# Performance work log

Measured on AMD Instinct MI355X. Metric: run time of the kernel, lower is better.

## Reference

```python
import jax, jax.numpy as jnp
import numpy as np

N_NODES = 100000
N_EDGES = 1600000
NODE_DIM = 128
HIDDEN_DIM = 128


def _sage_conv(x, src, dst, deg_inv, W_l, W_r, b):
    # PyG SAGEConv (aggr='mean', root_weight=True):
    #   out = lin_l(mean_{j in N(i)} x_j) + lin_r(x_i)
    msgs = x[src]                                             # [E, d_in] gather
    agg = jax.ops.segment_sum(msgs, dst, num_segments=N_NODES)  # [N, d_in]
    mean = agg * deg_inv[:, None]
    return mean @ W_l + x @ W_r + b


def setup_inputs() -> dict:
    key = jax.random.key(0)
    ks = jax.random.split(key, 9)
    x = jax.random.normal(ks[0], (N_NODES, NODE_DIM), dtype=jnp.float32)
    edge_index = jax.random.randint(ks[1], (2, N_EDGES), 0, N_NODES, dtype=jnp.int32)
    t = jnp.zeros((1,), dtype=jnp.float32)

    def glorot(k, fan_in, fan_out):
        s = (6.0 / (fan_in + fan_out)) ** 0.5
        return jax.random.uniform(k, (fan_in, fan_out), jnp.float32, -s, s)

    return {
        "t": t,
        "x": x,
        "edge_index": edge_index,
        "W1_l": glorot(ks[2], NODE_DIM, HIDDEN_DIM),
        "W1_r": glorot(ks[3], NODE_DIM, HIDDEN_DIM),
        "b1": jnp.zeros((HIDDEN_DIM,), jnp.float32),
        "W2_l": glorot(ks[4], HIDDEN_DIM, HIDDEN_DIM),
        "W2_r": glorot(ks[5], HIDDEN_DIM, HIDDEN_DIM),
        "b2": jnp.zeros((HIDDEN_DIM,), jnp.float32),
        "W3_l": glorot(ks[6], HIDDEN_DIM, NODE_DIM),
        "W3_r": glorot(ks[7], HIDDEN_DIM, NODE_DIM),
        "b3": jnp.zeros((NODE_DIM,), jnp.float32),
    }


def reference(t, x, edge_index, W1_l, W1_r, b1, W2_l, W2_r, b2, W3_l, W3_r, b3):
    src, dst = edge_index[0], edge_index[1]
    deg = jax.ops.segment_sum(jnp.ones((N_EDGES,), x.dtype), dst, num_segments=N_NODES)
    deg_inv = jnp.where(deg > 0, 1.0 / jnp.maximum(deg, 1.0), 0.0)

    h = jax.nn.relu(_sage_conv(x, src, dst, deg_inv, W1_l, W1_r, b1))
    h = jax.nn.relu(_sage_conv(h, src, dst, deg_inv, W2_l, W2_r, b2))
    dx_dt = _sage_conv(h, src, dst, deg_inv, W3_l, W3_r, b3)
    return dx_dt
```

## Files before the change

### kernel.cpp

```cpp
#include <hip/hip_runtime.h>

#define NN   100000
#define NE   1600000
#define DIM  128
#define NBKT 391
#define EPB  16384
#define NBLK 98
#define NTILES (NN / 16)
#define CASTB 12500
#define CWB   384


typedef short          s16x8 __attribute__((ext_vector_type(8)));
typedef unsigned short u16x8 __attribute__((ext_vector_type(8)));
typedef float          f32x4 __attribute__((ext_vector_type(4)));

__device__ __forceinline__ unsigned short f2b(float f) {
    unsigned u = __float_as_uint(f);
    unsigned r = ((u >> 16) & 1u) + 0x7FFFu;
    return (unsigned short)((u + r) >> 16);
}
__device__ __forceinline__ float b2f(unsigned short h) {
    return __uint_as_float(((unsigned)h) << 16);
}

__global__ void k_prep(const float* __restrict__ x, unsigned short* __restrict__ xb,
                       const int* __restrict__ dst, int* __restrict__ hist,
                       const float* __restrict__ W1l, const float* __restrict__ W1r,
                       const float* __restrict__ W2l, const float* __restrict__ W2r,
                       const float* __restrict__ W3l, const float* __restrict__ W3r,
                       unsigned short* __restrict__ Wt1, unsigned short* __restrict__ Wt2,
                       unsigned short* __restrict__ Wt3) {
    __shared__ int lh[NBKT];
    int t = threadIdx.x, b = blockIdx.x;
    if (b < NBLK) {
        for (int j = t; j < NBKT; j += 256) lh[j] = 0;
        __syncthreads();
        int base = b * EPB;
        int end = base + EPB; if (end > NE) end = NE;
        for (int i = base + t; i < end; i += 256) atomicAdd(&lh[dst[i] >> 8], 1);
        __syncthreads();
        for (int j = t; j < NBKT; j += 256) hist[j * NBLK + b] = lh[j];
    } else if (b < NBLK + CASTB) {
        int i = (b - NBLK) * 256 + t;
        float4 v = ((const float4*)x)[i];
        ushort4 o;
        o.x = f2b(v.x); o.y = f2b(v.y); o.z = f2b(v.z); o.w = f2b(v.w);
        ((ushort4*)xb)[i] = o;
    } else {
        int i = (b - NBLK - CASTB) * 256 + t;
        int L = i >> 15;
        int rem = i & 32767;
        int n = rem >> 8;
        int k = rem & 255;
        const float* Wl = (L == 0) ? W1l : (L == 1) ? W2l : W3l;
        const float* Wr = (L == 0) ? W1r : (L == 1) ? W2r : W3r;
        unsigned short* Wt = (L == 0) ? Wt1 : (L == 1) ? Wt2 : Wt3;
        float v = (k < 128) ? Wl[k * 128 + n] : Wr[(k - 128) * 128 + n];
        Wt[n * 256 + k] = f2b(v);
    }
}

__global__ void k_scanrow(int* __restrict__ hist, int* __restrict__ row_total) {
    __shared__ int sh[128];
    int k = blockIdx.x, t = threadIdx.x;
    int v = (t < NBLK) ? hist[k * NBLK + t] : 0;
    sh[t] = v;
    __syncthreads();
    for (int off = 1; off < 128; off <<= 1) {
        int a = (t >= off) ? sh[t - off] : 0;
        __syncthreads();
        sh[t] += a;
        __syncthreads();
    }
    if (t < NBLK) hist[k * NBLK + t] = sh[t] - v;
    if (t == 127) row_total[k] = sh[127];
}

__global__ void k_bin2(const int* __restrict__ src, const int* __restrict__ dst,
                       const int* __restrict__ hist, const int* __restrict__ row_total,
                       int* __restrict__ bbase, int* __restrict__ binned) {
    __shared__ int s_base[NBKT];
    __shared__ int s_cnt[NBKT];
    __shared__ int ps[256];
    int t = threadIdx.x, b = blockIdx.x;
    int a0 = (2 * t     < NBKT) ? row_total[2 * t]     : 0;
    int a1 = (2 * t + 1 < NBKT) ? row_total[2 * t + 1] : 0;
    ps[t] = a0 + a1;
    __syncthreads();
    for (int off = 1; off < 256; off <<= 1) {
        int v = (t >= off) ? ps[t - off] : 0;
        __syncthreads();
        ps[t] += v;
        __syncthreads();
    }
    int pe = ps[t] - (a0 + a1);
    if (2 * t     < NBKT) s_base[2 * t]     = pe;
    if (2 * t + 1 < NBKT) s_base[2 * t + 1] = pe + a0;
    __syncthreads();
    if (b == 0) {
        for (int j = t; j < NBKT; j += 256) bbase[j] = s_base[j];
        if (t == 0) bbase[NBKT] = NE;
    }
    for (int j = t; j < NBKT; j += 256) {
        s_base[j] += hist[j * NBLK + b];
        s_cnt[j] = 0;
    }
    __syncthreads();
    int base = b * EPB;
    int end = base + EPB; if (end > NE) end = NE;
    for (int i = base + t; i < end; i += 256) {
        int d = dst[i];
        int k = d >> 8;
        int w = (src[i] << 8) | (d & 255);
        int lpos = atomicAdd(&s_cnt[k], 1);
        binned[s_base[k] + lpos] = w;
    }
}

__global__ void k_build(const int* __restrict__ binned,
                        const int* __restrict__ bucket_base,
                        int* __restrict__ csr, int4* __restrict__ meta) {
    __shared__ int s_deg[256], s_scan[256], s_cur[256];
    __shared__ int stage[8192];
    int b = blockIdx.x, t = threadIdx.x;
    int base = bucket_base[b], end = bucket_base[b + 1];
    int cnt = end - base;
    s_deg[t] = 0;
    __syncthreads();
    for (int i = t; i < cnt; i += 256)
        atomicAdd(&s_deg[binned[base + i] & 255], 1);
    __syncthreads();
    s_scan[t] = s_deg[t];
    __syncthreads();
    for (int off = 1; off < 256; off <<= 1) {
        int a = (t >= off) ? s_scan[t - off] : 0;
        __syncthreads();
        s_scan[t] += a;
        __syncthreads();
    }
    int excl = s_scan[t] - s_deg[t];
    s_cur[t] = excl;
    int node = b * 256 + t;
    if (node < NN) {
        int d = s_deg[t];
        float di = (d > 0) ? 1.0f / (float)d : 0.0f;
        int4 M; M.x = base + excl; M.y = d; M.z = __float_as_int(di); M.w = 0;
        meta[node] = M;
    }
    __syncthreads();
    for (int i = t; i < cnt; i += 256) {
        int w = binned[base + i];
        int pos = atomicAdd(&s_cur[w & 255], 1);
        int s = w >> 8;
        if (pos < 8192) stage[pos] = s;
        else            csr[base + pos] = s;
    }
    __syncthreads();
    int m = cnt < 8192 ? cnt : 8192;
    for (int i = t; i < m; i += 256) csr[base + i] = stage[i];
}

__global__ void k_gather(const unsigned short* __restrict__ feat,
                         const int4* __restrict__ meta,
                         const int* __restrict__ csr,
                         unsigned short* __restrict__ mean) {
    int lane = threadIdx.x & 63;
    int wv   = threadIdx.x >> 6;
    int n    = blockIdx.x * 4 + wv;
    int q = lane >> 4, c = lane & 15;
    int4 M = meta[n];
    int base = M.x;
    int d    = M.y;
    float s  = __int_as_float(M.z);
    float acc0[8], acc1[8];
#pragma unroll
    for (int t = 0; t < 8; t++) { acc0[t] = 0.0f; acc1[t] = 0.0f; }
    const u16x8* fp = (const u16x8*)feat;
    int j = q;
    for (; j + 4 < d; j += 8) {
        int s0 = csr[base + j];
        int s1 = csr[base + j + 4];
        u16x8 v0 = fp[s0 * 16 + c];
        u16x8 v1 = fp[s1 * 16 + c];
#pragma unroll
        for (int t = 0; t < 8; t++) { acc0[t] += b2f(v0[t]); acc1[t] += b2f(v1[t]); }
    }
    if (j < d) {
        int s0 = csr[base + j];
        u16x8 v0 = fp[s0 * 16 + c];
#pragma unroll
        for (int t = 0; t < 8; t++) acc0[t] += b2f(v0[t]);
    }
#pragma unroll
    for (int t = 0; t < 8; t++) acc0[t] += acc1[t];
#pragma unroll
    for (int t = 0; t < 8; t++) {
        acc0[t] += __shfl_xor(acc0[t], 16, 64);
        acc0[t] += __shfl_xor(acc0[t], 32, 64);
    }
    if (q == 0) {
        u16x8 o;
#pragma unroll
        for (int t = 0; t < 8; t++) o[t] = f2b(acc0[t] * s);
        ((u16x8*)mean)[n * 16 + c] = o;
    }
}

template <int MODE>
__global__ void __launch_bounds__(512)
k_lin(const unsigned short* __restrict__ meanb,
      const unsigned short* __restrict__ hb,
      const unsigned short* __restrict__ Wt,
      const float* __restrict__ bias, void* __restrict__ out) {
    __shared__ s16x8 sW[4096];
    int t = threadIdx.x;
    const s16x8* wp = (const s16x8*)Wt;
#pragma unroll
    for (int it = 0; it < 8; it++) {
        int ci = it * 512 + t;
        int frag = ci >> 6, ln = ci & 63;
        int mt = frag >> 3, kt = frag & 7;
        int m = mt * 16 + (ln & 15);
        int kc = kt * 4 + (ln >> 4);
        sW[ci] = wp[m * 32 + kc];
    }
    __syncthreads();

    int lane = t & 63;
    int wv   = t >> 6;
    int tile = blockIdx.x * 8 + wv;
    if (tile >= NTILES) return;
    int n0 = tile * 16;
    int q = lane >> 4, c = lane & 15;
    const s16x8* mp = (const s16x8*)meanb;
    const s16x8* hp = (const s16x8*)hb;
    int row = n0 + c;
    s16x8 B[8];
#pragma unroll
    for (int kt = 0; kt < 4; kt++) B[kt] = mp[row * 16 + kt * 4 + q];
#pragma unroll
    for (int kt = 0; kt < 4; kt++) B[4 + kt] = hp[row * 16 + kt * 4 + q];
    const f32x4* bp = (const f32x4*)bias;
#pragma unroll
    for (int mt = 0; mt < 8; mt++) {
        f32x4 acc = {0.f, 0.f, 0.f, 0.f};
#pragma unroll
        for (int kt = 0; kt < 8; kt++)
            acc = __builtin_amdgcn_mfma_f32_16x16x32_bf16(sW[(mt * 8 + kt) * 64 + lane],
                                                          B[kt], acc, 0, 0, 0);
        f32x4 bv = bp[mt * 4 + q];
        int node = n0 + c;
        if (MODE == 0) {
            ushort4 o;
            float v0 = acc[0] + bv[0]; if (v0 < 0.f) v0 = 0.f;
            float v1 = acc[1] + bv[1]; if (v1 < 0.f) v1 = 0.f;
            float v2 = acc[2] + bv[2]; if (v2 < 0.f) v2 = 0.f;
            float v3 = acc[3] + bv[3]; if (v3 < 0.f) v3 = 0.f;
            o.x = f2b(v0); o.y = f2b(v1); o.z = f2b(v2); o.w = f2b(v3);
            ((ushort4*)out)[node * 32 + mt * 4 + q] = o;
        } else {
            f32x4 v;
#pragma unroll
            for (int r = 0; r < 4; r++) v[r] = acc[r] + bv[r];
            ((f32x4*)out)[node * 32 + mt * 4 + q] = v;
        }
    }
}

extern "C" void kernel_launch(void* const* d_in, const int* in_sizes, int n_in,
                              void* d_out, int out_size, void* d_ws, size_t ws_size,
                              hipStream_t stream) {
    const float* x   = (const float*)d_in[1];
    const int*   ei  = (const int*)d_in[2];
    const int*   src = ei;
    const int*   dst = ei + NE;
    const float* W1l = (const float*)d_in[3];
    const float* W1r = (const float*)d_in[4];
    const float* b1  = (const float*)d_in[5];
    const float* W2l = (const float*)d_in[6];
    const float* W2r = (const float*)d_in[7];
    const float* b2  = (const float*)d_in[8];
    const float* W3l = (const float*)d_in[9];
    const float* W3r = (const float*)d_in[10];
    const float* b3  = (const float*)d_in[11];

    char* w = (char*)d_ws;
    auto carve = [&](size_t bytes) {
        void* p = (void*)w;
        w += (bytes + 255) & ~(size_t)255;
        return p;
    };
    int4*  meta      = (int4*)carve((size_t)NN * 16);
    int*   hist      = (int*)carve((size_t)NBKT * NBLK * 4);
    int*   row_total = (int*)carve(NBKT * 4);
    int*   bbase     = (int*)carve((NBKT + 1) * 4);
    int*   csr       = (int*)carve((size_t)NE * 4);
    unsigned short* Wt1 = (unsigned short*)carve(128 * 256 * 2);
    unsigned short* Wt2 = (unsigned short*)carve(128 * 256 * 2);
    unsigned short* Wt3 = (unsigned short*)carve(128 * 256 * 2);
    unsigned short* xb    = (unsigned short*)carve((size_t)NN * DIM * 2);
    unsigned short* meanb = (unsigned short*)carve((size_t)NN * DIM * 2);
    unsigned short* h1b   = (unsigned short*)carve((size_t)NN * DIM * 2);
    unsigned short* h2b   = xb;
    int*   binned    = (int*)meanb;

    k_prep<<<NBLK + CASTB + CWB, 256, 0, stream>>>(x, xb, dst, hist,
                                                   W1l, W1r, W2l, W2r, W3l, W3r,
                                                   Wt1, Wt2, Wt3);
    k_scanrow<<<NBKT, 128, 0, stream>>>(hist, row_total);
    k_bin2<<<NBLK, 256, 0, stream>>>(src, dst, hist, row_total, bbase, binned);
    k_build<<<NBKT, 256, 0, stream>>>(binned, bbase, csr, meta);

    const int GB = NN / 4;
    const int LB = (NTILES + 7) / 8;

    k_gather<<<GB, 256, 0, stream>>>(xb, meta, csr, meanb);
    k_lin<0><<<LB, 512, 0, stream>>>(meanb, xb, Wt1, b1, (void*)h1b);
    k_gather<<<GB, 256, 0, stream>>>(h1b, meta, csr, meanb);
    k_lin<0><<<LB, 512, 0, stream>>>(meanb, h1b, Wt2, b2, (void*)h2b);
    k_gather<<<GB, 256, 0, stream>>>(h2b, meta, csr, meanb);
    k_lin<1><<<LB, 512, 0, stream>>>(meanb, h2b, Wt3, b3, d_out);
}
```

Measured before the change: 445.5 us.

## Fuse neighbor-mean gather with MFMA linear layer per 64-node block

Merges the separate gather and linear kernels into one kernel per layer. Each 1024-thread block gathers neighbor means for 64 nodes into swizzled shared memory, then runs MFMA on the mean and root features directly. This removes the global write and reread of the bf16 mean buffer and three kernel launches. In exchange, every block reloads the 64KB weight tile for only 64 nodes and the large blocks may limit occupancy.

Result: slower. 465.3 us (+4.4%).

```diff
diff --git a/kernel.cpp b/kernel.cpp
--- a/kernel.cpp
+++ b/kernel.cpp
@@ -6,9 +6,10 @@
 #define NBKT 391
 #define EPB  16384
 #define NBLK 98
-#define NTILES (NN / 16)
 #define CASTB 12500
 #define CWB   384
+#define FNB  64
+#define FGB  ((NN + FNB - 1) / FNB)
 
 
 typedef short          s16x8 __attribute__((ext_vector_type(8)));
@@ -161,96 +162,107 @@
     for (int i = t; i < m; i += 256) csr[base + i] = stage[i];
 }
 
-__global__ void k_gather(const unsigned short* __restrict__ feat,
-                         const int4* __restrict__ meta,
-                         const int* __restrict__ csr,
-                         unsigned short* __restrict__ mean) {
-    int lane = threadIdx.x & 63;
-    int wv   = threadIdx.x >> 6;
-    int n    = blockIdx.x * 4 + wv;
-    int q = lane >> 4, c = lane & 15;
-    int4 M = meta[n];
-    int base = M.x;
-    int d    = M.y;
-    float s  = __int_as_float(M.z);
-    float acc0[8], acc1[8];
-#pragma unroll
-    for (int t = 0; t < 8; t++) { acc0[t] = 0.0f; acc1[t] = 0.0f; }
-    const u16x8* fp = (const u16x8*)feat;
-    int j = q;
-    for (; j + 4 < d; j += 8) {
-        int s0 = csr[base + j];
-        int s1 = csr[base + j + 4];
-        u16x8 v0 = fp[s0 * 16 + c];
-        u16x8 v1 = fp[s1 * 16 + c];
-#pragma unroll
-        for (int t = 0; t < 8; t++) { acc0[t] += b2f(v0[t]); acc1[t] += b2f(v1[t]); }
-    }
-    if (j < d) {
-        int s0 = csr[base + j];
-        u16x8 v0 = fp[s0 * 16 + c];
-#pragma unroll
-        for (int t = 0; t < 8; t++) acc0[t] += b2f(v0[t]);
-    }
-#pragma unroll
-    for (int t = 0; t < 8; t++) acc0[t] += acc1[t];
-#pragma unroll
-    for (int t = 0; t < 8; t++) {
-        acc0[t] += __shfl_xor(acc0[t], 16, 64);
-        acc0[t] += __shfl_xor(acc0[t], 32, 64);
-    }
-    if (q == 0) {
-        u16x8 o;
-#pragma unroll
-        for (int t = 0; t < 8; t++) o[t] = f2b(acc0[t] * s);
-        ((u16x8*)mean)[n * 16 + c] = o;
-    }
-}
-
 template <int MODE>
-__global__ void __launch_bounds__(512)
-k_lin(const unsigned short* __restrict__ meanb,
-      const unsigned short* __restrict__ hb,
-      const unsigned short* __restrict__ Wt,
-      const float* __restrict__ bias, void* __restrict__ out) {
+__global__ void __launch_bounds__(1024, 8)
+k_gl(const unsigned short* __restrict__ feat,
+     const int4* __restrict__ meta, const int* __restrict__ csr,
+     const unsigned short* __restrict__ Wt,
+     const float* __restrict__ bias, void* __restrict__ out) {
     __shared__ s16x8 sW[4096];
+    __shared__ s16x8 sM[FNB * 16];
     int t = threadIdx.x;
     const s16x8* wp = (const s16x8*)Wt;
 #pragma unroll
-    for (int it = 0; it < 8; it++) {
-        int ci = it * 512 + t;
+    for (int it = 0; it < 4; it++) {
+        int ci = it * 1024 + t;
         int frag = ci >> 6, ln = ci & 63;
         int mt = frag >> 3, kt = frag & 7;
         int m = mt * 16 + (ln & 15);
         int kc = kt * 4 + (ln >> 4);
         sW[ci] = wp[m * 32 + kc];
     }
-    __syncthreads();
 
     int lane = t & 63;
     int wv   = t >> 6;
-    int tile = blockIdx.x * 8 + wv;
-    if (tile >= NTILES) return;
-    int n0 = tile * 16;
+    int n0   = blockIdx.x * FNB;
     int q = lane >> 4, c = lane & 15;
-    const s16x8* mp = (const s16x8*)meanb;
-    const s16x8* hp = (const s16x8*)hb;
-    int row = n0 + c;
-    s16x8 B[8];
-#pragma unroll
-    for (int kt = 0; kt < 4; kt++) B[kt] = mp[row * 16 + kt * 4 + q];
-#pragma unroll
-    for (int kt = 0; kt < 4; kt++) B[4 + kt] = hp[row * 16 + kt * 4 + q];
+    const u16x8* fp = (const u16x8*)feat;
+
+    for (int i = 0; i < 4; i++) {
+        int nb = wv * 4 + i;
+        int n  = n0 + nb;
+        if (n < NN) {
+            int4 M = meta[n];
+            int base = M.x;
+            int d    = M.y;
+            float s  = __int_as_float(M.z);
+            float acc0[8], acc1[8];
+#pragma unroll
+            for (int e = 0; e < 8; e++) { acc0[e] = 0.0f; acc1[e] = 0.0f; }
+            int j = q;
+            for (; j + 4 < d; j += 8) {
+                int s0 = csr[base + j];
+                int s1 = csr[base + j + 4];
+                u16x8 v0 = fp[s0 * 16 + c];
+                u16x8 v1 = fp[s1 * 16 + c];
+#pragma unroll
+                for (int e = 0; e < 8; e++) { acc0[e] += b2f(v0[e]); acc1[e] += b2f(v1[e]); }
+            }
+            if (j < d) {
+                int s0 = csr[base + j];
+                u16x8 v0 = fp[s0 * 16 + c];
+#pragma unroll
+                for (int e = 0; e < 8; e++) acc0[e] += b2f(v0[e]);
+            }
+#pragma unroll
+            for (int e = 0; e < 8; e++) acc0[e] += acc1[e];
+#pragma unroll
+            for (int e = 0; e < 8; e++) {
+                acc0[e] += __shfl_xor(acc0[e], 16, 64);
+                acc0[e] += __shfl_xor(acc0[e], 32, 64);
+            }
+            if (q == 0) {
+                u16x8 o;
+#pragma unroll
+                for (int e = 0; e < 8; e++) o[e] = f2b(acc0[e] * s);
+                ((u16x8*)sM)[nb * 16 + (c ^ (nb & 15))] = o;
+            }
+        }
+    }
+    __syncthreads();
+
+    const s16x8* hp = (const s16x8*)feat;
     const f32x4* bp = (const f32x4*)bias;
 #pragma unroll
-    for (int mt = 0; mt < 8; mt++) {
+    for (int s = 0; s < 2; s++) {
+        int task = wv * 2 + s;
+        int tile = task >> 3, mt = task & 7;
+        int tn0 = n0 + tile * 16;
+        if (tn0 + 15 >= NN) continue;
+        int c2 = lane & 15, q2 = lane >> 4;
+        int node = tn0 + c2;
         f32x4 acc = {0.f, 0.f, 0.f, 0.f};
-#pragma unroll
-        for (int kt = 0; kt < 8; kt++)
-            acc = __builtin_amdgcn_mfma_f32_16x16x32_bf16(sW[(mt * 8 + kt) * 64 + lane],
-                                                          B[kt], acc, 0, 0, 0);
-        f32x4 bv = bp[mt * 4 + q];
-        int node = n0 + c;
+        {
+            s16x8 B0 = sM[(tile * 16 + c2) * 16 + ((0 * 4 + q2) ^ c2)];
+            s16x8 B1 = sM[(tile * 16 + c2) * 16 + ((1 * 4 + q2) ^ c2)];
+            s16x8 B2 = sM[(tile * 16 + c2) * 16 + ((2 * 4 + q2) ^ c2)];
+            s16x8 B3 = sM[(tile * 16 + c2) * 16 + ((3 * 4 + q2) ^ c2)];
+            acc = __builtin_amdgcn_mfma_f32_16x16x32_bf16(sW[(mt * 8 + 0) * 64 + lane], B0, acc, 0, 0, 0);
+            acc = __builtin_amdgcn_mfma_f32_16x16x32_bf16(sW[(mt * 8 + 1) * 64 + lane], B1, acc, 0, 0, 0);
+            acc = __builtin_amdgcn_mfma_f32_16x16x32_bf16(sW[(mt * 8 + 2) * 64 + lane], B2, acc, 0, 0, 0);
+            acc = __builtin_amdgcn_mfma_f32_16x16x32_bf16(sW[(mt * 8 + 3) * 64 + lane], B3, acc, 0, 0, 0);
+        }
+        {
+            s16x8 B4 = hp[node * 16 + 0 * 4 + q2];
+            s16x8 B5 = hp[node * 16 + 1 * 4 + q2];
+            s16x8 B6 = hp[node * 16 + 2 * 4 + q2];
+            s16x8 B7 = hp[node * 16 + 3 * 4 + q2];
+            acc = __builtin_amdgcn_mfma_f32_16x16x32_bf16(sW[(mt * 8 + 4) * 64 + lane], B4, acc, 0, 0, 0);
+            acc = __builtin_amdgcn_mfma_f32_16x16x32_bf16(sW[(mt * 8 + 5) * 64 + lane], B5, acc, 0, 0, 0);
+            acc = __builtin_amdgcn_mfma_f32_16x16x32_bf16(sW[(mt * 8 + 6) * 64 + lane], B6, acc, 0, 0, 0);
+            acc = __builtin_amdgcn_mfma_f32_16x16x32_bf16(sW[(mt * 8 + 7) * 64 + lane], B7, acc, 0, 0, 0);
+        }
+        f32x4 bv = bp[mt * 4 + q2];
         if (MODE == 0) {
             ushort4 o;
             float v0 = acc[0] + bv[0]; if (v0 < 0.f) v0 = 0.f;
@@ -258,12 +270,12 @@
             float v2 = acc[2] + bv[2]; if (v2 < 0.f) v2 = 0.f;
             float v3 = acc[3] + bv[3]; if (v3 < 0.f) v3 = 0.f;
             o.x = f2b(v0); o.y = f2b(v1); o.z = f2b(v2); o.w = f2b(v3);
-            ((ushort4*)out)[node * 32 + mt * 4 + q] = o;
+            ((ushort4*)out)[node * 32 + mt * 4 + q2] = o;
         } else {
             f32x4 v;
 #pragma unroll
             for (int r = 0; r < 4; r++) v[r] = acc[r] + bv[r];
-            ((f32x4*)out)[node * 32 + mt * 4 + q] = v;
+            ((f32x4*)out)[node * 32 + mt * 4 + q2] = v;
         }
     }
 }
@@ -300,10 +312,9 @@
     unsigned short* Wt2 = (unsigned short*)carve(128 * 256 * 2);
     unsigned short* Wt3 = (unsigned short*)carve(128 * 256 * 2);
     unsigned short* xb    = (unsigned short*)carve((size_t)NN * DIM * 2);
-    unsigned short* meanb = (unsigned short*)carve((size_t)NN * DIM * 2);
     unsigned short* h1b   = (unsigned short*)carve((size_t)NN * DIM * 2);
     unsigned short* h2b   = xb;
-    int*   binned    = (int*)meanb;
+    int*   binned    = (int*)h1b;
 
     k_prep<<<NBLK + CASTB + CWB, 256, 0, stream>>>(x, xb, dst, hist,
                                                    W1l, W1r, W2l, W2r, W3l, W3r,
@@ -312,13 +323,7 @@
     k_bin2<<<NBLK, 256, 0, stream>>>(src, dst, hist, row_total, bbase, binned);
     k_build<<<NBKT, 256, 0, stream>>>(binned, bbase, csr, meta);
 
-    const int GB = NN / 4;
-    const int LB = (NTILES + 7) / 8;
-
-    k_gather<<<GB, 256, 0, stream>>>(xb, meta, csr, meanb);
-    k_lin<0><<<LB, 512, 0, stream>>>(meanb, xb, Wt1, b1, (void*)h1b);
-    k_gather<<<GB, 256, 0, stream>>>(h1b, meta, csr, meanb);
-    k_lin<0><<<LB, 512, 0, stream>>>(meanb, h1b, Wt2, b2, (void*)h2b);
-    k_gather<<<GB, 256, 0, stream>>>(h2b, meta, csr, meanb);
-    k_lin<1><<<LB, 512, 0, stream>>>(meanb, h2b, Wt3, b3, d_out);
-}
+    k_gl<0><<<FGB, 1024, 0, stream>>>(xb, meta, csr, Wt1, b1, (void*)h1b);
+    k_gl<0><<<FGB, 1024, 0, stream>>>(h1b, meta, csr, Wt2, b2, (void*)h2b);
+    k_gl<1><<<FGB, 1024, 0, stream>>>(h2b, meta, csr, Wt3, b3, d_out);
+}
```
